# Kernel tuning notes

Measured on AMD Instinct MI355X. Metric: run time of the kernel, lower is better.

Reference implementation:

```python
import jax, jax.numpy as jnp
import numpy as np

NUM_HEADS = 16
EPS = 1e-12  # softmax_2relu eps
MASK_VALUE = -1e9  # stands in for torch.finfo(dtype).min; relu zeroes it anyway


def setup_inputs() -> dict:
    key = jax.random.key(0)
    k1, k2, k3 = jax.random.split(key, 3)
    B, S, D = 4, 1024, 1024
    hidden_states = jax.random.normal(k1, (B, S, D), dtype=jnp.float32)
    c_attn_w = jax.random.normal(k2, (D, 3 * D), dtype=jnp.float32) * 0.02
    c_attn_b = jnp.zeros((3 * D,), dtype=jnp.float32)
    c_proj_w = jax.random.normal(k3, (D, D), dtype=jnp.float32) * 0.02
    c_proj_b = jnp.zeros((D,), dtype=jnp.float32)
    return {
        "hidden_states": hidden_states,
        "c_attn_w": c_attn_w,
        "c_attn_b": c_attn_b,
        "c_proj_w": c_proj_w,
        "c_proj_b": c_proj_b,
    }


def softmax_2relu(scores, axis=-1, eps=EPS):
    r = jax.nn.relu(scores)
    n = scores.shape[axis]
    return (r + eps / n) / (jnp.sum(r, axis=axis, keepdims=True) + eps)


def reference(hidden_states, c_attn_w, c_attn_b, c_proj_w, c_proj_b):
    B, S, D = hidden_states.shape
    H = NUM_HEADS
    dh = D // H

    # fused QKV projection (Conv1D: x @ W + b)
    qkv = hidden_states @ c_attn_w + c_attn_b  # [B, S, 3D]
    q, k, v = jnp.split(qkv, 3, axis=-1)

    def to_heads(t):
        return t.reshape(B, S, H, dh).transpose(0, 2, 1, 3)  # [B, H, S, dh]

    q, k, v = to_heads(q), to_heads(k), to_heads(v)

    # attention scores, scaled
    scores = jnp.einsum("bhqd,bhkd->bhqk", q, k) / jnp.sqrt(
        jnp.asarray(dh, dtype=hidden_states.dtype)
    )

    # causal mask: masked positions set to large negative (relu -> 0)
    causal = jnp.tril(jnp.ones((S, S), dtype=bool))
    scores = jnp.where(causal[None, None, :, :], scores, MASK_VALUE)

    # custom relu-softmax normalization (softmax_2relu)
    attn = softmax_2relu(scores, axis=-1)

    ctx = jnp.einsum("bhqk,bhkd->bhqd", attn, v)  # [B, H, S, dh]
    ctx = ctx.transpose(0, 2, 1, 3).reshape(B, S, D)

    out = ctx @ c_proj_w + c_proj_b
    return out
```

## Files before the change

kernel.cpp:

```cpp
#include <hip/hip_runtime.h>
#include <hip/hip_bf16.h>

typedef unsigned short u16;
typedef unsigned int u32;

#define AS1 __attribute__((address_space(1)))
#define AS3 __attribute__((address_space(3)))

typedef __attribute__((ext_vector_type(8))) __bf16 bf16x8;
typedef __attribute__((ext_vector_type(4))) float f32x4;
typedef __attribute__((ext_vector_type(8))) u16 u16x8;

static __device__ __forceinline__ u16 f2bf(float f) {
    u32 x = __builtin_bit_cast(u32, f);
    u32 r = (x + 0x7fffu + ((x >> 16) & 1u)) >> 16;
    return (u16)r;
}
static __device__ __forceinline__ float bf2f(u16 u) {
    u32 x = ((u32)u) << 16;
    return __builtin_bit_cast(float, x);
}
static __device__ __forceinline__ void gload_lds16(const void* g, void* l) {
    __builtin_amdgcn_global_load_lds((const AS1 u32*)g, (AS3 u32*)l, 16, 0, 0);
}
static __device__ __forceinline__ u32 cvtpk(float lo, float hi) {
    u32 r;
    asm("v_cvt_pk_bf16_f32 %0, %1, %2" : "=v"(r) : "v"(lo), "v"(hi));
    return r;
}

__global__ __launch_bounds__(256) void k_prep(const float* __restrict__ X,
                                              u16* __restrict__ Xb,
                                              const float* __restrict__ Wqkv,
                                              u16* __restrict__ Wqkvt,
                                              const float* __restrict__ Wproj,
                                              u16* __restrict__ Wprojt) {
    __shared__ u16 T[64][65];
    int bid = blockIdx.x, t = threadIdx.x;
    if (bid < 2048) {
        int i = bid * 256 + t;
        typedef __attribute__((ext_vector_type(4))) float fx4;
        const fx4* p = (const fx4*)X;
        fx4 a = p[2 * i], b = p[2 * i + 1];
        u16x8 o;
        o[0] = f2bf(a[0]); o[1] = f2bf(a[1]); o[2] = f2bf(a[2]); o[3] = f2bf(a[3]);
        o[4] = f2bf(b[0]); o[5] = f2bf(b[1]); o[6] = f2bf(b[2]); o[7] = f2bf(b[3]);
        *(u16x8*)(Xb + (size_t)i * 8) = o;
        return;
    }
    const float* W; u16* Wt; int N_, nt, kt;
    if (bid < 2816) {
        W = Wqkv; Wt = Wqkvt; N_ = 3072;
        int u = bid - 2048; nt = u % 48; kt = u / 48;
    } else {
        W = Wproj; Wt = Wprojt; N_ = 1024;
        int u = bid - 2816; nt = u & 15; kt = u >> 4;
    }
    int c = t & 63, r0 = t >> 6;
#pragma unroll
    for (int i = 0; i < 16; i++) {
        int k = r0 + i * 4;
        T[k][c] = f2bf(W[(size_t)(kt * 64 + k) * N_ + nt * 64 + c]);
    }
    __syncthreads();
#pragma unroll
    for (int i = 0; i < 16; i++) {
        int nn = r0 + i * 4;
        Wt[(size_t)(nt * 64 + nn) * 1024 + kt * 64 + c] = T[c][nn];
    }
}

template <int EPI>
__global__ __launch_bounds__(256, 2) void k_gemm(
    const u16* __restrict__ A, const u16* __restrict__ Bt,
    const float* __restrict__ bias, float* __restrict__ outf,
    u16* __restrict__ Qb, u16* __restrict__ Kb, u16* __restrict__ Vb,
    u16* __restrict__ Vt, float* __restrict__ vpart,
    int Msz, int Nsz, int Ksz) {
    __shared__ u16 Al[128 * 64];
    __shared__ u16 Bl[128 * 64];
    int tid = threadIdx.x;
    int m0 = blockIdx.x * 128, n0 = blockIdx.y * 128;
    int w = tid >> 6, lane = tid & 63, l15 = lane & 15, lg = lane >> 4;
    int wr = (w >> 1) * 64, wc = (w & 1) * 64;
    f32x4 acc[4][4] = {};

    for (int k0 = 0; k0 < Ksz; k0 += 64) {
#pragma unroll
        for (int i = 0; i < 4; i++) {
            int c = i * 256 + tid;
            gload_lds16(A + (size_t)(m0 + (c >> 3)) * Ksz + k0 + (c & 7) * 8,
                        &Al[(c & ~63) * 8]);
        }
#pragma unroll
        for (int i = 0; i < 4; i++) {
            int c = i * 256 + tid;
            gload_lds16(Bt + (size_t)(n0 + (c >> 3)) * Ksz + k0 + (c & 7) * 8,
                        &Bl[(c & ~63) * 8]);
        }
        __syncthreads();
#pragma unroll
        for (int kk = 0; kk < 2; kk++) {
            bf16x8 af[4], bfr[4];
#pragma unroll
            for (int m = 0; m < 4; m++)
                af[m] = *(const bf16x8*)&Al[(wr + m * 16 + l15) * 64 + kk * 32 + lg * 8];
#pragma unroll
            for (int n = 0; n < 4; n++)
                bfr[n] = *(const bf16x8*)&Bl[(wc + n * 16 + l15) * 64 + kk * 32 + lg * 8];
#pragma unroll
            for (int m = 0; m < 4; m++)
#pragma unroll
                for (int n = 0; n < 4; n++)
                    acc[m][n] = __builtin_amdgcn_mfma_f32_16x16x32_bf16(af[m], bfr[n], acc[m][n], 0, 0, 0);
        }
        __syncthreads();
    }

    if (EPI == 0) {
#pragma unroll
        for (int n = 0; n < 4; n++) {
            int gn = n0 + wc + n * 16 + l15;
            float bv = bias[gn];
#pragma unroll
            for (int m = 0; m < 4; m++) {
                int gmb = m0 + wr + m * 16 + lg * 4;
#pragma unroll
                for (int r = 0; r < 4; r++)
                    outf[(size_t)(gmb + r) * Nsz + gn] = acc[m][n][r] + bv;
            }
        }
    } else {
        u16* T = Al;
        const int TP = 136;
        float bv[4];
#pragma unroll
        for (int n = 0; n < 4; n++) bv[n] = bias[n0 + wc + n * 16 + l15];
        int lrow = tid >> 3;
        int c0 = (tid & 7) << 4;
        int gcol = n0 + c0;
        int which = gcol >> 10, d = gcol & 1023, h = d >> 6, dd = d & 63;
        u16* dstb = which == 0 ? Qb : (which == 1 ? Kb : Vb);
        bool isV = (n0 >= 2048);
        int s0 = m0 & 1023, bq = m0 >> 10;
        int dl = tid >> 1, sh = tid & 1;
        int bhV = bq * 16 + ((n0 - 2048) >> 6) + (dl >> 6);
        float vp0 = 0.f, vp1 = 0.f;

#define EPI_CHUNK(mc)                                                              \
    {                                                                              \
        __syncthreads();                                                           \
        if (((mc) >> 1) == (w >> 1)) {                                             \
            _Pragma("unroll") for (int n = 0; n < 4; n++) {                        \
                _Pragma("unroll") for (int r = 0; r < 4; r++) {                    \
                    int lr = (lg << 2) + r;                                        \
                    T[lr * TP + wc + (n << 4) + l15] =                             \
                        f2bf(acc[2 * ((mc) & 1)][n][r] + bv[n]);                   \
                    T[(16 + lr) * TP + wc + (n << 4) + l15] =                      \
                        f2bf(acc[2 * ((mc) & 1) + 1][n][r] + bv[n]);               \
                }                                                                  \
            }                                                                      \
        }                                                                          \
        __syncthreads();                                                           \
        if (!isV) {                                                                \
            int gm = m0 + (mc) * 32 + lrow;                                        \
            int b = gm >> 10, s = gm & 1023;                                       \
            u16* dp = dstb + ((size_t)(b * 16 + h) * 1024 + s) * 64 + dd;          \
            const u16* sp = &T[lrow * TP + c0];                                    \
            *(u16x8*)dp = *(const u16x8*)sp;                                       \
            *(u16x8*)(dp + 8) = *(const u16x8*)(sp + 8);                           \
        } else {                                                                   \
            if ((mc) == 0 && s0 == 0) {                                            \
                u16* dp = dstb + ((size_t)(bq * 16 + h) * 1024 + lrow) * 64 + dd;  \
                const u16* sp = &T[lrow * TP + c0];                                \
                *(u16x8*)dp = *(const u16x8*)sp;                                   \
                *(u16x8*)(dp + 8) = *(const u16x8*)(sp + 8);                       \
            }                                                                      \
            float vls = 0.f;                                                       \
            u16x8 o0, o1;                                                          \
            _Pragma("unroll") for (int r = 0; r < 8; r++) {                        \
                u16 v = T[((sh << 4) + r) * TP + dl];                              \
                o0[r] = v; vls += bf2f(v);                                         \
            }                                                                      \
            _Pragma("unroll") for (int r = 0; r < 8; r++) {                        \
                u16 v = T[((sh << 4) + 8 + r) * TP + dl];                          \
                o1[r] = v; vls += bf2f(v);                                         \
            }                                                                      \
            vls += __shfl_xor(vls, 1);                                             \
            if ((mc) < 2) vp0 += vls; else vp1 += vls;                             \
            u16* vtp = Vt + (size_t)bhV * 65536 + (size_t)(dl & 63) * 1024 +       \
                       s0 + (mc) * 32 + (sh << 4);                                 \
            *(u16x8*)vtp = o0;                                                     \
            *(u16x8*)(vtp + 8) = o1;                                               \
        }                                                                          \
    }

        EPI_CHUNK(0) EPI_CHUNK(1) EPI_CHUNK(2) EPI_CHUNK(3)
#undef EPI_CHUNK

        if (isV && sh == 0) {
            int st0 = s0 >> 6;
            vpart[((size_t)bhV * 16 + st0) * 64 + (dl & 63)] = vp0;
            vpart[((size_t)bhV * 16 + st0 + 1) * 64 + (dl & 63)] = vp1;
        }
    }
}

__global__ __launch_bounds__(256, 2) void k_gemmP(
    const u16* __restrict__ A, const u16* __restrict__ Bt,
    const float* __restrict__ bias, float* __restrict__ outf) {
    __shared__ u16 Al[128 * 64];
    __shared__ u16 Bl[64 * 64];
    int tid = threadIdx.x;
    int m0 = blockIdx.x * 128, n0 = blockIdx.y * 64;
    int w = tid >> 6, lane = tid & 63, l15 = lane & 15, lg = lane >> 4;
    int wr = (w >> 1) * 64, wc = (w & 1) * 32;
    f32x4 acc[4][2] = {};

    for (int k0 = 0; k0 < 1024; k0 += 64) {
#pragma unroll
        for (int i = 0; i < 4; i++) {
            int c = i * 256 + tid;
            gload_lds16(A + (size_t)(m0 + (c >> 3)) * 1024 + k0 + (c & 7) * 8,
                        &Al[(c & ~63) * 8]);
        }
#pragma unroll
        for (int i = 0; i < 2; i++) {
            int c = i * 256 + tid;
            gload_lds16(Bt + (size_t)(n0 + (c >> 3)) * 1024 + k0 + (c & 7) * 8,
                        &Bl[(c & ~63) * 8]);
        }
        __syncthreads();
#pragma unroll
        for (int kk = 0; kk < 2; kk++) {
            bf16x8 af[4], bfr[2];
#pragma unroll
            for (int m = 0; m < 4; m++)
                af[m] = *(const bf16x8*)&Al[(wr + m * 16 + l15) * 64 + kk * 32 + lg * 8];
#pragma unroll
            for (int n = 0; n < 2; n++)
                bfr[n] = *(const bf16x8*)&Bl[(wc + n * 16 + l15) * 64 + kk * 32 + lg * 8];
#pragma unroll
            for (int m = 0; m < 4; m++)
#pragma unroll
                for (int n = 0; n < 2; n++)
                    acc[m][n] = __builtin_amdgcn_mfma_f32_16x16x32_bf16(af[m], bfr[n], acc[m][n], 0, 0, 0);
        }
        __syncthreads();
    }
#pragma unroll
    for (int n = 0; n < 2; n++) {
        int gn = n0 + wc + n * 16 + l15;
        float bv = bias[gn];
#pragma unroll
        for (int m = 0; m < 4; m++) {
            int gmb = m0 + wr + m * 16 + lg * 4;
#pragma unroll
            for (int r = 0; r < 4; r++)
                outf[(size_t)(gmb + r) * 1024 + gn] = acc[m][n][r] + bv;
        }
    }
}

__global__ __launch_bounds__(256) void k_vsum2(const float* __restrict__ vpart,
                                               float* __restrict__ vsum) {
    int idx = blockIdx.x * 256 + threadIdx.x;
    int bh = idx >> 6, d = idx & 63;
    const float* p = vpart + (size_t)bh * 1024 + d;
    float s = 0.f;
#pragma unroll
    for (int st = 0; st < 16; st++) s += p[st * 64];
    vsum[idx] = s;
}

__global__ __launch_bounds__(512, 4) void k_attn(const u16* __restrict__ Qb,
                                                 const u16* __restrict__ Kb,
                                                 const u16* __restrict__ Vt,
                                                 const float* __restrict__ vsum,
                                                 u16* __restrict__ ctx) {
    __shared__ u16 Kl[2][4096];
    __shared__ u16 Vl[2][4096];
    __shared__ u16 Pl[8 * 1024];
    __shared__ float rsw[8][16];
    int tid = threadIdx.x, w = tid >> 6, lane = tid & 63, l15 = lane & 15, lg = lane >> 4;
    int p = blockIdx.x;
    int tb = 7 - (p >> 6);
    int bh = p & 63;
    int qb = tb * 128 + w * 16;
    int nkb = 2 * tb + 2;
    int klast = (qb + 15) >> 6;

    const u16* Qh = Qb + (size_t)bh * 65536;
    const u16* Kh = Kb + (size_t)bh * 65536;
    const u16* Vh = Vt + (size_t)bh * 65536;
    u16* Pw = &Pl[w * 1024];
    int swz = (l15 & 7) << 4;
    int q = qb + l15;

    bf16x8 qf[2];
#pragma unroll
    for (int kk = 0; kk < 2; kk++)
        qf[kk] = *(const bf16x8*)(Qh + (size_t)q * 64 + kk * 32 + lg * 8);
    float vs[4];
#pragma unroll
    for (int n = 0; n < 4; n++) vs[n] = vsum[bh * 64 + n * 16 + l15];

    int srow = tid >> 3, schunk = tid & 7;
    int soff = ((schunk * 16) ^ ((srow & 7) << 4)) >> 1;
    u16* kdst = &Kl[0][0] + w * 512;
    u16* vdst = &Vl[0][0] + w * 512;

    f32x4 ctxa[4] = {};
    float rsp = 0.f;
    int cur = 0;

    gload_lds16(Kh + (size_t)srow * 64 + soff, kdst);
    gload_lds16(Vh + (size_t)srow * 1024 + soff, vdst);
    __syncthreads();

    for (int kb = 0; kb < nkb; kb++) {
        if (kb + 1 < nkb) {
            int nx = cur ^ 1;
            gload_lds16(Kh + (size_t)(((kb + 1) << 6) + srow) * 64 + soff,
                        &Kl[nx][0] + w * 512);
            gload_lds16(Vh + (size_t)srow * 1024 + ((kb + 1) << 6) + soff,
                        &Vl[nx][0] + w * 512);
        }
        if (kb <= klast) {
            bool masked = (kb == klast);
            const char* Kc = (const char*)&Kl[cur][0];
            const char* Vc = (const char*)&Vl[cur][0];
            f32x4 sc[4] = {};
            __builtin_amdgcn_s_setprio(1);
#pragma unroll
            for (int kk = 0; kk < 2; kk++)
#pragma unroll
                for (int n = 0; n < 4; n++) {
                    bf16x8 kf = *(const bf16x8*)(Kc + ((((n * 16 + l15) << 7) + (kk << 6) + (lg << 4)) ^ swz));
                    sc[n] = __builtin_amdgcn_mfma_f32_16x16x32_bf16(kf, qf[kk], sc[n], 0, 0, 0);
                }
            __builtin_amdgcn_s_setprio(0);
            int qml = q - (kb << 6) - (lg << 2);
#pragma unroll
            for (int n = 0; n < 4; n++) {
                float v0 = fmaxf(sc[n][0] * 0.125f, 0.f);
                float v1 = fmaxf(sc[n][1] * 0.125f, 0.f);
                float v2 = fmaxf(sc[n][2] * 0.125f, 0.f);
                float v3 = fmaxf(sc[n][3] * 0.125f, 0.f);
                if (masked) {
                    int c = qml - n * 16;
                    v0 = (0 <= c) ? v0 : 0.f;
                    v1 = (1 <= c) ? v1 : 0.f;
                    v2 = (2 <= c) ? v2 : 0.f;
                    v3 = (3 <= c) ? v3 : 0.f;
                }
                rsp += (v0 + v1) + (v2 + v3);
                u32 w0 = cvtpk(v0, v1), w1 = cvtpk(v2, v3);
                int base = l15 * 128 + n * 32 + lg * 8;
                *(u32*)((char*)Pw + ((base) ^ swz)) = w0;
                *(u32*)((char*)Pw + ((base + 4) ^ swz)) = w1;
            }
            bf16x8 pf0 = *(const bf16x8*)((char*)Pw + ((l15 * 128 + lg * 16) ^ swz));
            bf16x8 pf1 = *(const bf16x8*)((char*)Pw + ((l15 * 128 + 64 + lg * 16) ^ swz));
            __builtin_amdgcn_s_setprio(1);
#pragma unroll
            for (int n = 0; n < 4; n++) {
                bf16x8 vf = *(const bf16x8*)(Vc + ((((n * 16 + l15) << 7) + (lg << 4)) ^ swz));
                ctxa[n] = __builtin_amdgcn_mfma_f32_16x16x32_bf16(pf0, vf, ctxa[n], 0, 0, 0);
            }
#pragma unroll
            for (int n = 0; n < 4; n++) {
                bf16x8 vf = *(const bf16x8*)(Vc + ((((n * 16 + l15) << 7) + 64 + (lg << 4)) ^ swz));
                ctxa[n] = __builtin_amdgcn_mfma_f32_16x16x32_bf16(pf1, vf, ctxa[n], 0, 0, 0);
            }
            __builtin_amdgcn_s_setprio(0);
        }
        __syncthreads();
        cur ^= 1;
    }

    float tsum = rsp;
    tsum += __shfl_xor(tsum, 16);
    tsum += __shfl_xor(tsum, 32);
    rsw[w][l15] = tsum;
    f32x4 rv = *(f32x4*)&rsw[w][lg * 4];
    const float EPS = 1e-12f, EPSN = 1e-12f / 1024.f;
    float inv[4];
#pragma unroll
    for (int r = 0; r < 4; r++) inv[r] = 1.f / (rv[r] + EPS);
    int b = bh >> 4, h = bh & 15;
#pragma unroll
    for (int n = 0; n < 4; n++) {
#pragma unroll
        for (int r = 0; r < 4; r++) {
            int qq = qb + lg * 4 + r;
            float val = (ctxa[n][r] + EPSN * vs[n]) * inv[r];
            ctx[(size_t)(b * 1024 + qq) * 1024 + h * 64 + n * 16 + l15] = f2bf(val);
        }
    }
}

__global__ __launch_bounds__(256) void k_qkfix(const float* __restrict__ X,
                                               const float* __restrict__ W,
                                               const float* __restrict__ bias,
                                               float* __restrict__ Qf,
                                               float* __restrict__ Kf) {
    __shared__ float red[4][8][64];
    int cb = blockIdx.x;
    int b = blockIdx.y >> 1, rh = blockIdx.y & 1;
    int tid = threadIdx.x, w = tid >> 6, lane = tid & 63;
    int col = cb * 64 + lane;

    const float* Wp = W + (size_t)(w * 256) * 3072 + col;
    const float* Xp = X + ((size_t)b * 1024 + rh * 8) * 1024 + w * 256;
    float acc[8] = {};
#pragma unroll 8
    for (int it = 0; it < 256; ++it) {
        float wv = Wp[(size_t)it * 3072];
#pragma unroll
        for (int j = 0; j < 8; j++) acc[j] += Xp[(size_t)j * 1024 + it] * wv;
    }
#pragma unroll
    for (int j = 0; j < 8; j++) red[w][j][lane] = acc[j];
    __syncthreads();

    int isK = cb >> 4, h = cb & 15;
    float* dst = isK ? Kf : Qf;
#pragma unroll
    for (int o = tid; o < 512; o += 256) {
        int j = o >> 6, c = o & 63;
        float s = red[0][j][c] + red[1][j][c] + red[2][j][c] + red[3][j][c];
        dst[((size_t)(b * 16 + h) * 16 + rh * 8 + j) * 64 + c] = s + bias[cb * 64 + c];
    }
}

__global__ __launch_bounds__(256) void k_attnfix(const float* __restrict__ Qf,
                                                 const float* __restrict__ Kf,
                                                 const u16* __restrict__ Vb,
                                                 const float* __restrict__ vsum,
                                                 u16* __restrict__ ctx) {
    __shared__ float ps[16][17];
    __shared__ float dens[16];
    int bh = blockIdx.x, t = threadIdx.x;
    int q = t >> 4, k = t & 15;
    const float* Qr = Qf + ((size_t)bh * 16 + q) * 64;
    const float* Kr = Kf + ((size_t)bh * 16 + k) * 64;
    float s = 0.f;
    for (int d = 0; d < 64; d++) s += Qr[d] * Kr[d];
    s *= 0.125f;
    float p = (k <= q) ? fmaxf(s, 0.f) : 0.f;
    float den = p;
    den += __shfl_xor(den, 1); den += __shfl_xor(den, 2);
    den += __shfl_xor(den, 4); den += __shfl_xor(den, 8);
    ps[q][k] = p;
    if (k == 0) dens[q] = den;
    __syncthreads();
    int d0 = (t & 15) * 4;
    float c[4] = {};
    for (int kk = 0; kk <= q; kk++) {
        float pv = ps[q][kk];
        const u16* vr = Vb + ((size_t)bh * 1024 + kk) * 64 + d0;
        c[0] += pv * bf2f(vr[0]); c[1] += pv * bf2f(vr[1]);
        c[2] += pv * bf2f(vr[2]); c[3] += pv * bf2f(vr[3]);
    }
    float inv = 1.f / (dens[q] + 1e-12f);
    const float EPSN = 1e-12f / 1024.f;
    const float* vs = vsum + bh * 64 + d0;
    int b = bh >> 4, h = bh & 15;
    u16* dst = ctx + (size_t)(b * 1024 + q) * 1024 + h * 64 + d0;
#pragma unroll
    for (int j = 0; j < 4; j++) dst[j] = f2bf((c[j] + EPSN * vs[j]) * inv);
}

extern "C" void kernel_launch(void* const* d_in, const int* in_sizes, int n_in,
                              void* d_out, int out_size, void* d_ws, size_t ws_size,
                              hipStream_t stream) {
    const float* X = (const float*)d_in[0];
    const float* Wqkv = (const float*)d_in[1];
    const float* bqkv = (const float*)d_in[2];
    const float* Wproj = (const float*)d_in[3];
    const float* bproj = (const float*)d_in[4];
    float* out = (float*)d_out;
    char* ws = (char*)d_ws;

    u16* Xb     = (u16*)(ws);
    u16* Wqkvt  = (u16*)(ws + 8388608);
    u16* Wprojt = (u16*)(ws + 14680064);
    u16* Qb     = (u16*)(ws + 16777216);
    u16* Kb     = (u16*)(ws + 25165824);
    u16* Vb     = (u16*)(ws + 33554432);
    u16* Vt     = (u16*)(ws + 41943040);
    float* vsum = (float*)(ws + 50331648);
    float* Qf   = (float*)(ws + 50348032);
    float* Kf   = (float*)(ws + 50610176);
    float* vpart= (float*)(ws + 50872320);
    u16* ctx    = Xb;

    k_prep<<<dim3(3072), dim3(256), 0, stream>>>(X, Xb, Wqkv, Wqkvt, Wproj, Wprojt);
    k_gemm<1><<<dim3(32, 24), dim3(256), 0, stream>>>(Xb, Wqkvt, bqkv, nullptr,
                                                      Qb, Kb, Vb, Vt, vpart,
                                                      4096, 3072, 1024);
    k_vsum2<<<dim3(16), dim3(256), 0, stream>>>(vpart, vsum);
    k_qkfix<<<dim3(32, 8), dim3(256), 0, stream>>>(X, Wqkv, bqkv, Qf, Kf);
    k_attn<<<dim3(512), dim3(512), 0, stream>>>(Qb, Kb, Vt, vsum, ctx);
    k_attnfix<<<dim3(64), dim3(256), 0, stream>>>(Qf, Kf, Vb, vsum, ctx);
    k_gemmP<<<dim3(32, 16), dim3(256), 0, stream>>>(ctx, Wprojt, bproj, out);
}
```

Measured before the change: 127.2 us.

## Fold qkfix, vsum and attnfix kernels into prep and attention launches

The fp32 fix-up projection for the first 16 query/key rows moves into extra blocks of the prep kernel. The V column-sum reduction is now computed per block inside the attention kernel instead of in its own kernel. The first-rows attention fix-up runs as 64 extra blocks of the attention kernel, and the main path skips writing those rows. This cuts seven launches to four and removes the serialization gaps between small kernels, at the cost of redundantly re-summing vpart in every attention block and adding shared memory.

```diff
diff --git a/kernel.cpp b/kernel.cpp
--- a/kernel.cpp
+++ b/kernel.cpp
@@ -34,27 +34,58 @@
                                               const float* __restrict__ Wqkv,
                                               u16* __restrict__ Wqkvt,
                                               const float* __restrict__ Wproj,
-                                              u16* __restrict__ Wprojt) {
+                                              u16* __restrict__ Wprojt,
+                                              const float* __restrict__ bqkv,
+                                              float* __restrict__ Qf,
+                                              float* __restrict__ Kf) {
     __shared__ u16 T[64][65];
+    __shared__ float red[4][8][64];
     int bid = blockIdx.x, t = threadIdx.x;
-    if (bid < 2048) {
-        int i = bid * 256 + t;
+    if (bid < 256) {
+        int cb = bid >> 3, y = bid & 7;
+        int b = y >> 1, rh = y & 1;
+        int w = t >> 6, lane = t & 63;
+        int col = cb * 64 + lane;
+        const float* Wp = Wqkv + (size_t)(w * 256) * 3072 + col;
+        const float* Xp = X + ((size_t)b * 1024 + rh * 8) * 1024 + w * 256;
+        float acc[8] = {};
+#pragma unroll 8
+        for (int it = 0; it < 256; ++it) {
+            float wv = Wp[(size_t)it * 3072];
+#pragma unroll
+            for (int j = 0; j < 8; j++) acc[j] += Xp[(size_t)j * 1024 + it] * wv;
+        }
+#pragma unroll
+        for (int j = 0; j < 8; j++) red[w][j][lane] = acc[j];
+        __syncthreads();
+        int isK = cb >> 4, h = cb & 15;
+        float* dst = isK ? Kf : Qf;
+#pragma unroll
+        for (int o = t; o < 512; o += 256) {
+            int j = o >> 6, c = o & 63;
+            float s = red[0][j][c] + red[1][j][c] + red[2][j][c] + red[3][j][c];
+            dst[((size_t)(b * 16 + h) * 16 + rh * 8 + j) * 64 + c] = s + bqkv[cb * 64 + c];
+        }
+        return;
+    }
+    if (bid < 2304) {
+        int i = (bid - 256) * 256 + t;
         typedef __attribute__((ext_vector_type(4))) float fx4;
         const fx4* p = (const fx4*)X;
-        fx4 a = p[2 * i], b = p[2 * i + 1];
+        fx4 a = p[2 * i], bb = p[2 * i + 1];
         u16x8 o;
         o[0] = f2bf(a[0]); o[1] = f2bf(a[1]); o[2] = f2bf(a[2]); o[3] = f2bf(a[3]);
-        o[4] = f2bf(b[0]); o[5] = f2bf(b[1]); o[6] = f2bf(b[2]); o[7] = f2bf(b[3]);
+        o[4] = f2bf(bb[0]); o[5] = f2bf(bb[1]); o[6] = f2bf(bb[2]); o[7] = f2bf(bb[3]);
         *(u16x8*)(Xb + (size_t)i * 8) = o;
         return;
     }
     const float* W; u16* Wt; int N_, nt, kt;
-    if (bid < 2816) {
+    if (bid < 3072) {
         W = Wqkv; Wt = Wqkvt; N_ = 3072;
-        int u = bid - 2048; nt = u % 48; kt = u / 48;
+        int u = bid - 2304; nt = u % 48; kt = u / 48;
     } else {
         W = Wproj; Wt = Wprojt; N_ = 1024;
-        int u = bid - 2816; nt = u & 15; kt = u >> 4;
+        int u = bid - 3072; nt = u & 15; kt = u >> 4;
     }
     int c = t & 63, r0 = t >> 6;
 #pragma unroll
@@ -262,28 +293,67 @@
     }
 }
 
-__global__ __launch_bounds__(256) void k_vsum2(const float* __restrict__ vpart,
-                                               float* __restrict__ vsum) {
-    int idx = blockIdx.x * 256 + threadIdx.x;
-    int bh = idx >> 6, d = idx & 63;
-    const float* p = vpart + (size_t)bh * 1024 + d;
-    float s = 0.f;
-#pragma unroll
-    for (int st = 0; st < 16; st++) s += p[st * 64];
-    vsum[idx] = s;
-}
-
 __global__ __launch_bounds__(512, 4) void k_attn(const u16* __restrict__ Qb,
                                                  const u16* __restrict__ Kb,
                                                  const u16* __restrict__ Vt,
-                                                 const float* __restrict__ vsum,
+                                                 const float* __restrict__ vpart,
+                                                 const u16* __restrict__ Vb,
+                                                 const float* __restrict__ Qf,
+                                                 const float* __restrict__ Kf,
                                                  u16* __restrict__ ctx) {
     __shared__ u16 Kl[2][4096];
     __shared__ u16 Vl[2][4096];
     __shared__ u16 Pl[8 * 1024];
     __shared__ float rsw[8][16];
+    __shared__ float vsl[64];
+    __shared__ float ps[16][17];
+    __shared__ float dens[16];
     int tid = threadIdx.x, w = tid >> 6, lane = tid & 63, l15 = lane & 15, lg = lane >> 4;
     int p = blockIdx.x;
+
+    if (p >= 512) {
+        int bhf = p - 512;
+        if (tid < 64) {
+            float s = 0.f;
+            const float* pp = vpart + (size_t)bhf * 1024 + tid;
+#pragma unroll
+            for (int st = 0; st < 16; st++) s += pp[st * 64];
+            vsl[tid] = s;
+        }
+        int q = tid >> 4, k = tid & 15;
+        if (tid < 256) {
+            const float* Qr = Qf + ((size_t)bhf * 16 + q) * 64;
+            const float* Kr = Kf + ((size_t)bhf * 16 + k) * 64;
+            float s = 0.f;
+            for (int d = 0; d < 64; d++) s += Qr[d] * Kr[d];
+            s *= 0.125f;
+            float pv = (k <= q) ? fmaxf(s, 0.f) : 0.f;
+            float den = pv;
+            den += __shfl_xor(den, 1); den += __shfl_xor(den, 2);
+            den += __shfl_xor(den, 4); den += __shfl_xor(den, 8);
+            ps[q][k] = pv;
+            if (k == 0) dens[q] = den;
+        }
+        __syncthreads();
+        if (tid < 256) {
+            int d0 = k * 4;
+            float c[4] = {};
+            for (int kk = 0; kk <= q; kk++) {
+                float pv = ps[q][kk];
+                const u16* vr = Vb + ((size_t)bhf * 1024 + kk) * 64 + d0;
+                c[0] += pv * bf2f(vr[0]); c[1] += pv * bf2f(vr[1]);
+                c[2] += pv * bf2f(vr[2]); c[3] += pv * bf2f(vr[3]);
+            }
+            float inv = 1.f / (dens[q] + 1e-12f);
+            const float EPSN = 1e-12f / 1024.f;
+            int b = bhf >> 4, h = bhf & 15;
+            u16* dst = ctx + (size_t)(b * 1024 + q) * 1024 + h * 64 + d0;
+#pragma unroll
+            for (int j = 0; j < 4; j++) dst[j] = f2bf((c[j] + EPSN * vsl[d0 + j]) * inv);
+        }
+        return;
+    }
+
     int tb = 7 - (p >> 6);
     int bh = p & 63;
     int qb = tb * 128 + w * 16;
@@ -301,9 +371,6 @@
 #pragma unroll
     for (int kk = 0; kk < 2; kk++)
         qf[kk] = *(const bf16x8*)(Qh + (size_t)q * 64 + kk * 32 + lg * 8);
-    float vs[4];
-#pragma unroll
-    for (int n = 0; n < 4; n++) vs[n] = vsum[bh * 64 + n * 16 + l15];
 
     int srow = tid >> 3, schunk = tid & 7;
     int soff = ((schunk * 16) ^ ((srow & 7) << 4)) >> 1;
@@ -316,7 +383,17 @@
 
     gload_lds16(Kh + (size_t)srow * 64 + soff, kdst);
     gload_lds16(Vh + (size_t)srow * 1024 + soff, vdst);
+    if (tid < 64) {
+        float s = 0.f;
+        const float* pp = vpart + (size_t)bh * 1024 + tid;
+#pragma unroll
+        for (int st = 0; st < 16; st++) s += pp[st * 64];
+        vsl[tid] = s;
+    }
     __syncthreads();
+    float vs[4];
+#pragma unroll
+    for (int n = 0; n < 4; n++) vs[n] = vsl[n * 16 + l15];
 
     for (int kb = 0; kb < nkb; kb++) {
         if (kb + 1 < nkb) {
@@ -388,88 +465,18 @@
     float inv[4];
 #pragma unroll
     for (int r = 0; r < 4; r++) inv[r] = 1.f / (rv[r] + EPS);
-    int b = bh >> 4, h = bh & 15;
-#pragma unroll
-    for (int n = 0; n < 4; n++) {
-#pragma unroll
-        for (int r = 0; r < 4; r++) {
-            int qq = qb + lg * 4 + r;
-            float val = (ctxa[n][r] + EPSN * vs[n]) * inv[r];
-            ctx[(size_t)(b * 1024 + qq) * 1024 + h * 64 + n * 16 + l15] = f2bf(val);
-        }
-    }
-}
-
-__global__ __launch_bounds__(256) void k_qkfix(const float* __restrict__ X,
-                                               const float* __restrict__ W,
-                                               const float* __restrict__ bias,
-                                               float* __restrict__ Qf,
-                                               float* __restrict__ Kf) {
-    __shared__ float red[4][8][64];
-    int cb = blockIdx.x;
-    int b = blockIdx.y >> 1, rh = blockIdx.y & 1;
-    int tid = threadIdx.x, w = tid >> 6, lane = tid & 63;
-    int col = cb * 64 + lane;
-
-    const float* Wp = W + (size_t)(w * 256) * 3072 + col;
-    const float* Xp = X + ((size_t)b * 1024 + rh * 8) * 1024 + w * 256;
-    float acc[8] = {};
-#pragma unroll 8
-    for (int it = 0; it < 256; ++it) {
-        float wv = Wp[(size_t)it * 3072];
-#pragma unroll
-        for (int j = 0; j < 8; j++) acc[j] += Xp[(size_t)j * 1024 + it] * wv;
-    }
-#pragma unroll
-    for (int j = 0; j < 8; j++) red[w][j][lane] = acc[j];
-    __syncthreads();
-
-    int isK = cb >> 4, h = cb & 15;
-    float* dst = isK ? Kf : Qf;
-#pragma unroll
-    for (int o = tid; o < 512; o += 256) {
-        int j = o >> 6, c = o & 63;
-        float s = red[0][j][c] + red[1][j][c] + red[2][j][c] + red[3][j][c];
-        dst[((size_t)(b * 16 + h) * 16 + rh * 8 + j) * 64 + c] = s + bias[cb * 64 + c];
-    }
-}
-
-__global__ __launch_bounds__(256) void k_attnfix(const float* __restrict__ Qf,
-                                                 const float* __restrict__ Kf,
-                                                 const u16* __restrict__ Vb,
-                                                 const float* __restrict__ vsum,
-                                                 u16* __restrict__ ctx) {
-    __shared__ float ps[16][17];
-    __shared__ float dens[16];
-    int bh = blockIdx.x, t = threadIdx.x;
-    int q = t >> 4, k = t & 15;
-    const float* Qr = Qf + ((size_t)bh * 16 + q) * 64;
-    const float* Kr = Kf + ((size_t)bh * 16 + k) * 64;
-    float s = 0.f;
-    for (int d = 0; d < 64; d++) s += Qr[d] * Kr[d];
-    s *= 0.125f;
-    float p = (k <= q) ? fmaxf(s, 0.f) : 0.f;
-    float den = p;
-    den += __shfl_xor(den, 1); den += __shfl_xor(den, 2);
-    den += __shfl_xor(den, 4); den += __shfl_xor(den, 8);
-    ps[q][k] = p;
-    if (k == 0) dens[q] = den;
-    __syncthreads();
-    int d0 = (t & 15) * 4;
-    float c[4] = {};
-    for (int kk = 0; kk <= q; kk++) {
-        float pv = ps[q][kk];
-        const u16* vr = Vb + ((size_t)bh * 1024 + kk) * 64 + d0;
-        c[0] += pv * bf2f(vr[0]); c[1] += pv * bf2f(vr[1]);
-        c[2] += pv * bf2f(vr[2]); c[3] += pv * bf2f(vr[3]);
-    }
-    float inv = 1.f / (dens[q] + 1e-12f);
-    const float EPSN = 1e-12f / 1024.f;
-    const float* vs = vsum + bh * 64 + d0;
-    int b = bh >> 4, h = bh & 15;
-    u16* dst = ctx + (size_t)(b * 1024 + q) * 1024 + h * 64 + d0;
-#pragma unroll
-    for (int j = 0; j < 4; j++) dst[j] = f2bf((c[j] + EPSN * vs[j]) * inv);
+    if (qb != 0) {
+        int b = bh >> 4, h = bh & 15;
+#pragma unroll
+        for (int n = 0; n < 4; n++) {
+#pragma unroll
+            for (int r = 0; r < 4; r++) {
+                int qq = qb + lg * 4 + r;
+                float val = (ctxa[n][r] + EPSN * vs[n]) * inv[r];
+                ctx[(size_t)(b * 1024 + qq) * 1024 + h * 64 + n * 16 + l15] = f2bf(val);
+            }
+        }
+    }
 }
 
 extern "C" void kernel_launch(void* const* d_in, const int* in_sizes, int n_in,
@@ -490,19 +497,16 @@
     u16* Kb     = (u16*)(ws + 25165824);
     u16* Vb     = (u16*)(ws + 33554432);
     u16* Vt     = (u16*)(ws + 41943040);
-    float* vsum = (float*)(ws + 50331648);
     float* Qf   = (float*)(ws + 50348032);
     float* Kf   = (float*)(ws + 50610176);
     float* vpart= (float*)(ws + 50872320);
     u16* ctx    = Xb;
 
-    k_prep<<<dim3(3072), dim3(256), 0, stream>>>(X, Xb, Wqkv, Wqkvt, Wproj, Wprojt);
+    k_prep<<<dim3(3328), dim3(256), 0, stream>>>(X, Xb, Wqkv, Wqkvt, Wproj, Wprojt,
+                                                 bqkv, Qf, Kf);
     k_gemm<1><<<dim3(32, 24), dim3(256), 0, stream>>>(Xb, Wqkvt, bqkv, nullptr,
                                                       Qb, Kb, Vb, Vt, vpart,
                                                       4096, 3072, 1024);
-    k_vsum2<<<dim3(16), dim3(256), 0, stream>>>(vpart, vsum);
-    k_qkfix<<<dim3(32, 8), dim3(256), 0, stream>>>(X, Wqkv, bqkv, Qf, Kf);
-    k_attn<<<dim3(512), dim3(512), 0, stream>>>(Qb, Kb, Vt, vsum, ctx);
-    k_attnfix<<<dim3(64), dim3(256), 0, stream>>>(Qf, Kf, Vb, vsum, ctx);
+    k_attn<<<dim3(576), dim3(512), 0, stream>>>(Qb, Kb, Vt, vpart, Vb, Qf, Kf, ctx);
     k_gemmP<<<dim3(32, 16), dim3(256), 0, stream>>>(ctx, Wprojt, bproj, out);
 }
```

Measured after the change: 116.1 us. 1.1x faster.
